# Optimization experiments

Hardware: AMD Instinct MI355X
Metric: run time of the kernel (lower is better)

## Reference

```python
import jax, jax.numpy as jnp
import numpy as np
from jax import lax

NPOINT, RADIUS, NSAMPLE, EPS = 2048, 0.1, 32, 1e-5


def setup_inputs() -> dict:
    key = jax.random.key(0)
    ks = jax.random.split(key, 8)
    B, N, D, CIN, COUT, DEPTH = 4, 8192, 29, 32, 64, 2
    return {
        "xyz": jax.random.uniform(ks[0], (B, 3, N), jnp.float32),
        "points": jax.random.normal(ks[1], (B, D, N), jnp.float32),
        "proj_w": jax.random.normal(ks[2], (COUT, CIN), jnp.float32) * 0.05,
        "proj_g": jnp.ones((COUT,), jnp.float32),
        "proj_b": jnp.zeros((COUT,), jnp.float32),
        "w1": jax.random.normal(ks[3], (DEPTH, COUT, COUT), jnp.float32) * 0.05,
        "g1": jnp.ones((DEPTH, COUT), jnp.float32),
        "b1": jnp.zeros((DEPTH, COUT), jnp.float32),
        "w2": jax.random.normal(ks[4], (DEPTH, COUT, COUT), jnp.float32) * 0.05,
        "g2": jnp.ones((DEPTH, COUT), jnp.float32),
        "b2": jnp.zeros((DEPTH, COUT), jnp.float32),
    }


def fps(xyz, npoint):
    # xyz: [B,N,3] -> idx [B,npoint]; deterministic start at index 0
    B, N, _ = xyz.shape
    def body(carry, _):
        dist, far = carry  # [B,N], [B]
        centroid = jnp.take_along_axis(xyz, far[:, None, None], axis=1)  # [B,1,3]
        d = jnp.sum((xyz - centroid) ** 2, -1)
        dist = jnp.minimum(dist, d)
        return (dist, jnp.argmax(dist, -1).astype(jnp.int32)), far
    init = (jnp.full((B, N), 1e10, xyz.dtype), jnp.zeros((B,), jnp.int32))
    _, idx = lax.scan(body, init, None, length=npoint)
    return jnp.transpose(idx)  # [B,npoint]


def ball_query(radius, nsample, xyz, new_xyz):
    # matches torch query_ball_point: invalid -> N, sort, take first nsample, backfill
    N = xyz.shape[1]
    sqr = (jnp.sum(new_xyz ** 2, -1)[:, :, None]
           + jnp.sum(xyz ** 2, -1)[:, None, :]
           - 2.0 * jnp.einsum("bsc,bnc->bsn", new_xyz, xyz))  # [B,S,N]
    cand = jnp.where(sqr <= radius * radius, jnp.arange(N, dtype=jnp.int32), jnp.int32(N))
    neg, _ = lax.top_k(-cand, nsample)
    idx = -neg  # nsample smallest indices, ascending
    first = idx[:, :, :1]
    return jnp.where(idx == N, first, idx)  # [B,S,K]


def gather_nb(p, idx):
    # p [B,N,C], idx [B,S,K] -> [B,S,K,C]
    return jax.vmap(lambda pb, ib: pb[ib])(p, idx)


def _conv(x, w):
    # 1x1 conv: w [O,C], x [B,C,K,S]
    return jnp.einsum("oc,bcks->boks", w, x)


def _bn(x, g, b):
    # training-mode BatchNorm2d over (B,K,S) per channel
    m = jnp.mean(x, (0, 2, 3), keepdims=True)
    v = jnp.var(x, (0, 2, 3), keepdims=True)
    return g[None, :, None, None] * (x - m) * lax.rsqrt(v + EPS) + b[None, :, None, None]


def reference(xyz, points, proj_w, proj_g, proj_b, w1, g1, b1, w2, g2, b2):
    xyz_t = jnp.transpose(xyz, (0, 2, 1))      # [B,N,3]
    pts_t = jnp.transpose(points, (0, 2, 1))   # [B,N,D]
    fidx = fps(xyz_t, NPOINT)                  # [B,S]
    new_xyz = jnp.take_along_axis(xyz_t, fidx[:, :, None], axis=1)  # [B,S,3]
    idx = ball_query(RADIUS, NSAMPLE, xyz_t, new_xyz)               # [B,S,K]
    grouped_xyz = gather_nb(xyz_t, idx) - new_xyz[:, :, None, :]    # [B,S,K,3]
    grouped_pts = gather_nb(pts_t, idx)                             # [B,S,K,D]
    new_points = jnp.concatenate([grouped_xyz, grouped_pts], -1)    # [B,S,K,3+D]
    x = jnp.transpose(new_points, (0, 3, 2, 1))                     # [B,C,K,S]
    x = jax.nn.relu(_bn(_conv(x, proj_w), proj_g, proj_b))
    for d in range(w1.shape[0]):
        idn = x
        x = jax.nn.relu(_bn(_conv(x, w1[d]), g1[d], b1[d]))
        x = _bn(_conv(x, w2[d]), g2[d], b2[d])
        x = jax.nn.relu(x + idn)
    feat = jnp.max(x, axis=2)                  # [B,Cout,S]
    return jnp.transpose(new_xyz, (0, 2, 1)), feat
```

## Files before the change

kernel.cpp:

```cpp
#include <hip/hip_runtime.h>
#include <cstdint>
#include <cstddef>

#define NPTS    8192
#define NPT     2048
#define KNB     32
#define NB      4
#define DPTS    29
#define CINP    32
#define CO      64
#define KS      (KNB*NPT)
#define TELEM   ((size_t)NB*CO*KS)
#define MCNT    262144.0f
#define BNEPS   1e-5f
#define FTHR    512
#define FWAVES  (FTHR/64)
#define FPT     16

typedef float v2f __attribute__((ext_vector_type(2)));

#define FPS_PAIR(P, A, B)                                                     \
    {                                                                         \
        v2f dx_, dy_, dz_, xx_, yy_, zz_, ss_, dd_;                           \
        asm("v_pk_add_f32 %0, %1, %2" : "=v"(dx_) : "v"(px##P), "v"(ncx));    \
        asm("v_pk_add_f32 %0, %1, %2" : "=v"(dy_) : "v"(py##P), "v"(ncy));    \
        asm("v_pk_add_f32 %0, %1, %2" : "=v"(dz_) : "v"(pz##P), "v"(ncz));    \
        asm("v_pk_mul_f32 %0, %1, %1" : "=v"(xx_) : "v"(dx_));                \
        asm("v_pk_mul_f32 %0, %1, %1" : "=v"(yy_) : "v"(dy_));                \
        asm("v_pk_mul_f32 %0, %1, %1" : "=v"(zz_) : "v"(dz_));                \
        asm("v_pk_add_f32 %0, %1, %2" : "=v"(ss_) : "v"(xx_), "v"(yy_));      \
        asm("v_pk_add_f32 %0, %1, %2" : "=v"(dd_) : "v"(ss_), "v"(zz_));      \
        d##A = fminf(d##A, dd_.x);                                            \
        d##B = fminf(d##B, dd_.y);                                            \
    }

static __device__ __forceinline__ unsigned long long umax64(unsigned long long a,
                                                            unsigned long long b) {
    return a > b ? a : b;
}

__global__ __launch_bounds__(FTHR) void fps_kernel(const float* __restrict__ xyz,
                                                   float* __restrict__ out0) {
    const int b = blockIdx.x;
    const int t = threadIdx.x;
    const int lane = t & 63;
    const int wid  = t >> 6;
    const float* xb = xyz + (size_t)b * 3 * NPTS;
    const int base = t * FPT;

    extern __shared__ float smem[];
    float* sx = smem;
    float* sy = sx + NPTS;
    float* sz = sy + NPTS;
    float* sc = sz + NPTS;
    unsigned long long* skey = (unsigned long long*)(sc + 3 * NPT);

    v2f px0,px1,px2,px3,px4,px5,px6,px7;
    v2f py0,py1,py2,py3,py4,py5,py6,py7;
    v2f pz0,pz1,pz2,pz3,pz4,pz5,pz6,pz7;
    float d0,d1,d2,d3,d4,d5,d6,d7,d8,d9,d10,d11,d12,d13,d14,d15;
    {
        const float4* x4 = (const float4*)(xb + base);
        const float4* y4 = (const float4*)(xb + NPTS + base);
        const float4* z4 = (const float4*)(xb + 2 * NPTS + base);
        float4* lx4 = (float4*)(sx + base);
        float4* ly4 = (float4*)(sy + base);
        float4* lz4 = (float4*)(sz + base);
        float4 v;
        v = x4[0]; lx4[0] = v; px0 = (v2f){v.x, v.y}; px1 = (v2f){v.z, v.w};
        v = x4[1]; lx4[1] = v; px2 = (v2f){v.x, v.y}; px3 = (v2f){v.z, v.w};
        v = x4[2]; lx4[2] = v; px4 = (v2f){v.x, v.y}; px5 = (v2f){v.z, v.w};
        v = x4[3]; lx4[3] = v; px6 = (v2f){v.x, v.y}; px7 = (v2f){v.z, v.w};
        v = y4[0]; ly4[0] = v; py0 = (v2f){v.x, v.y}; py1 = (v2f){v.z, v.w};
        v = y4[1]; ly4[1] = v; py2 = (v2f){v.x, v.y}; py3 = (v2f){v.z, v.w};
        v = y4[2]; ly4[2] = v; py4 = (v2f){v.x, v.y}; py5 = (v2f){v.z, v.w};
        v = y4[3]; ly4[3] = v; py6 = (v2f){v.x, v.y}; py7 = (v2f){v.z, v.w};
        v = z4[0]; lz4[0] = v; pz0 = (v2f){v.x, v.y}; pz1 = (v2f){v.z, v.w};
        v = z4[1]; lz4[1] = v; pz2 = (v2f){v.x, v.y}; pz3 = (v2f){v.z, v.w};
        v = z4[2]; lz4[2] = v; pz4 = (v2f){v.x, v.y}; pz5 = (v2f){v.z, v.w};
        v = z4[3]; lz4[3] = v; pz6 = (v2f){v.x, v.y}; pz7 = (v2f){v.z, v.w};
        d0=d1=d2=d3=d4=d5=d6=d7=d8=d9=d10=d11=d12=d13=d14=d15 = 1e10f;
    }

    float cx = xb[0], cy = xb[NPTS], cz = xb[2 * NPTS];
    float* ob = out0 + (size_t)b * 3 * NPT;
    if (t == 0) { sc[0] = cx; sc[NPT] = cy; sc[2 * NPT] = cz; }

    for (int i = 1; i < NPT; ++i) {
        const v2f ncx = (v2f){-cx, -cx};
        const v2f ncy = (v2f){-cy, -cy};
        const v2f ncz = (v2f){-cz, -cz};
        FPS_PAIR(0, 0, 1)   FPS_PAIR(1, 2, 3)
        FPS_PAIR(2, 4, 5)   FPS_PAIR(3, 6, 7)
        FPS_PAIR(4, 8, 9)   FPS_PAIR(5, 10, 11)
        FPS_PAIR(6, 12, 13) FPS_PAIR(7, 14, 15)

        float m0 = fmaxf(fmaxf(d0,  d1),  d2);
        float m1 = fmaxf(fmaxf(d3,  d4),  d5);
        float m2 = fmaxf(fmaxf(d6,  d7),  d8);
        float m3 = fmaxf(fmaxf(d9,  d10), d11);
        float m4 = fmaxf(fmaxf(d12, d13), d14);
        float u0 = fmaxf(fmaxf(m0, m1), m2);
        float u1 = fmaxf(fmaxf(m3, m4), d15);
        float tb = fmaxf(u0, u1);

        unsigned q0 = ((d0  == tb) ? 0x0001u : 0u) | ((d1  == tb) ? 0x0002u : 0u);
        unsigned q1 = ((d2  == tb) ? 0x0004u : 0u) | ((d3  == tb) ? 0x0008u : 0u);
        unsigned q2 = ((d4  == tb) ? 0x0010u : 0u) | ((d5  == tb) ? 0x0020u : 0u);
        unsigned q3 = ((d6  == tb) ? 0x0040u : 0u) | ((d7  == tb) ? 0x0080u : 0u);
        unsigned q4 = ((d8  == tb) ? 0x0100u : 0u) | ((d9  == tb) ? 0x0200u : 0u);
        unsigned q5 = ((d10 == tb) ? 0x0400u : 0u) | ((d11 == tb) ? 0x0800u : 0u);
        unsigned q6 = ((d12 == tb) ? 0x1000u : 0u) | ((d13 == tb) ? 0x2000u : 0u);
        unsigned q7 = ((d14 == tb) ? 0x4000u : 0u) | ((d15 == tb) ? 0x8000u : 0u);
        unsigned mk = (q0 | q1) | (q2 | q3) | (q4 | q5) | (q6 | q7);
        const int jj = __builtin_ctz(mk);
        const int gidx = base + jj;

        float r = tb;
        asm volatile(
            "s_nop 1\n\t"
            "v_max_f32 %0, %0, %0 row_shr:1\n\t"
            "s_nop 1\n\t"
            "v_max_f32 %0, %0, %0 row_shr:2\n\t"
            "s_nop 1\n\t"
            "v_max_f32 %0, %0, %0 row_shr:4\n\t"
            "s_nop 1\n\t"
            "v_max_f32 %0, %0, %0 row_shr:8\n\t"
            "s_nop 1\n\t"
            "v_max_f32 %0, %0, %0 row_bcast:15 row_mask:0xa\n\t"
            "s_nop 1\n\t"
            "v_max_f32 %0, %0, %0 row_bcast:31 row_mask:0xc\n\t"
            "s_nop 1"
            : "+v"(r));
        const float wm = __uint_as_float(
            (unsigned int)__builtin_amdgcn_readlane((int)__float_as_uint(r), 63));

        unsigned long long eq = __ballot(tb == wm);
        const int lwin = __ffsll((long long)eq) - 1;
        const int wgid = __builtin_amdgcn_readlane(gidx, lwin);

        const int par = i & 1;
        if (lane == 0)
            skey[par * FWAVES + wid] =
                (((unsigned long long)__float_as_uint(wm)) << 32) |
                (unsigned int)(~(unsigned int)wgid);
        __syncthreads();

        const ulonglong2* sk2 = (const ulonglong2*)(skey + par * FWAVES);
        ulonglong2 k01 = sk2[0], k23 = sk2[1], k45 = sk2[2], k67 = sk2[3];
        unsigned long long ka = umax64(k01.x, k01.y);
        unsigned long long kb = umax64(k23.x, k23.y);
        unsigned long long kc = umax64(k45.x, k45.y);
        unsigned long long kd = umax64(k67.x, k67.y);
        unsigned long long kbest = umax64(umax64(ka, kb), umax64(kc, kd));
        const int widx = (int)(~(unsigned int)kbest);

        cx = sx[widx]; cy = sy[widx]; cz = sz[widx];
        if (t == 0) { sc[i] = cx; sc[NPT + i] = cy; sc[2 * NPT + i] = cz; }
    }

    __syncthreads();
    const float4* s4 = (const float4*)sc;
    float4* o4 = (float4*)ob;
#pragma unroll
    for (int k = 0; k < 3; ++k) o4[t + k * FTHR] = s4[t + k * FTHR];
}

__global__ __launch_bounds__(256) void ballq_kernel(const float* __restrict__ xyz,
                                                    const float* __restrict__ out0,
                                                    int* __restrict__ idx) {
    const int gw   = (blockIdx.x * 256 + threadIdx.x) >> 6;
    const int lane = threadIdx.x & 63;
    const int b  = gw >> 11;
    const int si = gw & 2047;
    const float* xb = xyz + (size_t)b * 3 * NPTS;

    const float cx = out0[b * 3 * NPT + si];
    const float cy = out0[b * 3 * NPT + NPT + si];
    const float cz = out0[b * 3 * NPT + 2*NPT + si];
    const float csum = __fadd_rn(__fadd_rn(__fmul_rn(cx, cx), __fmul_rn(cy, cy)),
                                 __fmul_rn(cz, cz));
    const float R2 = (float)(0.1 * 0.1);

    __shared__ int buf[4][KNB];
    int* mybuf = buf[threadIdx.x >> 6];

    int cnt = 0;
    for (int n0 = 0; n0 < NPTS && cnt < KNB; n0 += 64) {
        const int i = n0 + lane;
        float pxv = xb[i], pyv = xb[NPTS + i], pzv = xb[2 * NPTS + i];
        float ps = __fadd_rn(__fadd_rn(__fmul_rn(pxv, pxv), __fmul_rn(pyv, pyv)),
                             __fmul_rn(pzv, pzv));
        float dot = __fmaf_rn(pzv, cz, __fmaf_rn(pyv, cy, __fmul_rn(pxv, cx)));
        float sqr = __fsub_rn(__fadd_rn(csum, ps), __fadd_rn(dot, dot));
        bool hit = (sqr <= R2);
        unsigned long long m = __ballot(hit);
        int pos = cnt + __popcll(m & ((1ull << lane) - 1ull));
        if (hit && pos < KNB) mybuf[pos] = i;
        cnt += __popcll(m);
    }
    int c = cnt < KNB ? cnt : KNB;
    int first = (cnt > 0) ? mybuf[0] : 0;
    if (lane < KNB) {
        int v = (lane < c) ? mybuf[lane] : first;
        idx[((size_t)gw << 5) + lane] = v;
    }
}

__global__ __launch_bounds__(256) void proj_kernel(const float* __restrict__ xyz,
                                                   const float* __restrict__ points,
                                                   const float* __restrict__ out0,
                                                   const int* __restrict__ idx,
                                                   const float* __restrict__ W,
                                                   float* __restrict__ out,
                                                   float* __restrict__ stats) {
    const int p = blockIdx.x * 256 + threadIdx.x;
    const int b = p >> 16;
    const int q = p & 65535;
    const int k = q >> 11;
    const int s = q & 2047;
    const int tid = threadIdx.x;

    __shared__ float ssum[CO], ssq[CO];
    if (tid < CO) { ssum[tid] = 0.f; ssq[tid] = 0.f; }
    __syncthreads();

    const int j = idx[((size_t)(b * NPT + s) << 5) + k];
    const float* xb = xyz + (size_t)b * 3 * NPTS;
    float a[CINP];
    a[0] = xb[j]            - out0[b * 3 * NPT + s];
    a[1] = xb[NPTS + j]     - out0[b * 3 * NPT + NPT + s];
    a[2] = xb[2*NPTS + j]   - out0[b * 3 * NPT + 2*NPT + s];
    const float* pb = points + (size_t)b * DPTS * NPTS;
#pragma unroll
    for (int c = 0; c < DPTS; ++c) a[3 + c] = pb[c * NPTS + j];

    const size_t obase = (size_t)b * CO * KS + q;
    for (int o = 0; o < CO; ++o) {
        float acc = 0.f;
#pragma unroll
        for (int c = 0; c < CINP; ++c) acc = __fmaf_rn(W[o * CINP + c], a[c], acc);
        out[obase + (size_t)o * KS] = acc;
        float s1 = acc, s2 = acc * acc;
#pragma unroll
        for (int off = 32; off > 0; off >>= 1) {
            s1 += __shfl_xor(s1, off, 64);
            s2 += __shfl_xor(s2, off, 64);
        }
        if ((tid & 63) == 0) { atomicAdd(&ssum[o], s1); atomicAdd(&ssq[o], s2); }
    }
    __syncthreads();
    if (tid < CO) {
        atomicAdd(&stats[tid], ssum[tid]);
        atomicAdd(&stats[CO + tid], ssq[tid]);
    }
}

template <bool HAS_IDN, bool WRITE_ACT>
__global__ __launch_bounds__(256) void conv_bn_kernel(const float* in,
                                                      const float* idn,
                                                      const float* __restrict__ stats_in,
                                                      const float* __restrict__ gamma,
                                                      const float* __restrict__ beta,
                                                      const float* __restrict__ W,
                                                      float* act_out,
                                                      float* out,
                                                      float* __restrict__ stats_out) {
    const int p = blockIdx.x * 256 + threadIdx.x;
    const int b = p >> 16;
    const int q = p & 65535;
    const int tid = threadIdx.x;

    __shared__ float ssc[CO], ssh[CO], ssum[CO], ssq[CO];
    if (tid < CO) {
        const float Minv = 1.0f / MCNT;
        float m = stats_in[tid] * Minv;
        float v = stats_in[CO + tid] * Minv - m * m;
        float scl = gamma[tid] * rsqrtf(v + BNEPS);
        ssc[tid] = scl;
        ssh[tid] = beta[tid] - m * scl;
        ssum[tid] = 0.f; ssq[tid] = 0.f;
    }
    __syncthreads();

    const size_t base = (size_t)b * CO * KS + q;
    float a[CO];
#pragma unroll
    for (int c = 0; c < CO; ++c) {
        float v = __fmaf_rn(ssc[c], in[base + (size_t)c * KS], ssh[c]);
        if (HAS_IDN) v += idn[base + (size_t)c * KS];
        v = fmaxf(v, 0.0f);
        a[c] = v;
        if (WRITE_ACT) act_out[base + (size_t)c * KS] = v;
    }
    for (int o = 0; o < CO; ++o) {
        float acc = 0.f;
#pragma unroll
        for (int c = 0; c < CO; ++c) acc = __fmaf_rn(W[o * CO + c], a[c], acc);
        out[base + (size_t)o * KS] = acc;
        float s1 = acc, s2 = acc * acc;
#pragma unroll
        for (int off = 32; off > 0; off >>= 1) {
            s1 += __shfl_xor(s1, off, 64);
            s2 += __shfl_xor(s2, off, 64);
        }
        if ((tid & 63) == 0) { atomicAdd(&ssum[o], s1); atomicAdd(&ssq[o], s2); }
    }
    __syncthreads();
    if (tid < CO) {
        atomicAdd(&stats_out[tid], ssum[tid]);
        atomicAdd(&stats_out[CO + tid], ssq[tid]);
    }
}

__global__ __launch_bounds__(256) void final_kernel(const float* __restrict__ y2,
                                                    const float* __restrict__ idn,
                                                    const float* __restrict__ stats,
                                                    const float* __restrict__ gamma,
                                                    const float* __restrict__ beta,
                                                    float* __restrict__ feat) {
    const int p = blockIdx.x * 256 + threadIdx.x;
    const int s = p & 2047;
    const int o = (p >> 11) & 63;
    const int b = p >> 17;
    const float Minv = 1.0f / MCNT;
    float m = stats[o] * Minv;
    float v = stats[CO + o] * Minv - m * m;
    float scl = gamma[o] * rsqrtf(v + BNEPS);
    float sh  = beta[o] - m * scl;
    const size_t base = (size_t)b * CO * KS + (size_t)o * KS + s;
    float mx = -1e30f;
#pragma unroll
    for (int k = 0; k < KNB; ++k) {
        float val = __fmaf_rn(scl, y2[base + (size_t)k * NPT], sh) + idn[base + (size_t)k * NPT];
        val = fmaxf(val, 0.0f);
        mx = fmaxf(mx, val);
    }
    feat[p] = mx;
}

__global__ void zero_kernel(float* p, int n) {
    int i = blockIdx.x * blockDim.x + threadIdx.x;
    if (i < n) p[i] = 0.f;
}

extern "C" void kernel_launch(void* const* d_in, const int* in_sizes, int n_in,
                              void* d_out, int out_size, void* d_ws, size_t ws_size,
                              hipStream_t stream) {
    (void)in_sizes; (void)n_in; (void)out_size; (void)ws_size;
    const float* xyz    = (const float*)d_in[0];
    const float* points = (const float*)d_in[1];
    const float* proj_w = (const float*)d_in[2];
    const float* proj_g = (const float*)d_in[3];
    const float* proj_b = (const float*)d_in[4];
    const float* w1     = (const float*)d_in[5];
    const float* g1     = (const float*)d_in[6];
    const float* b1     = (const float*)d_in[7];
    const float* w2     = (const float*)d_in[8];
    const float* g2     = (const float*)d_in[9];
    const float* b2     = (const float*)d_in[10];

    float* out0 = (float*)d_out;
    float* feat = (float*)d_out + NB * 3 * NPT;

    float* stats = (float*)d_ws;
    int*   idx   = (int*)((float*)d_ws + 1024);
    float* A     = (float*)(idx + NB * NPT * KNB);
    float* B     = A + TELEM;

    const size_t fps_lds = (size_t)(3 * NPTS + 3 * NPT) * sizeof(float)
                         + 2 * FWAVES * sizeof(unsigned long long);

    hipLaunchKernelGGL(zero_kernel, dim3(3), dim3(256), 0, stream, stats, 5 * 2 * CO);
    hipLaunchKernelGGL(fps_kernel, dim3(NB), dim3(FTHR), fps_lds, stream, xyz, out0);
    hipLaunchKernelGGL(ballq_kernel, dim3(2048), dim3(256), 0, stream, xyz, out0, idx);
    hipLaunchKernelGGL(proj_kernel, dim3(1024), dim3(256), 0, stream,
                       xyz, points, out0, idx, proj_w, A, stats);
    hipLaunchKernelGGL((conv_bn_kernel<false, true>), dim3(1024), dim3(256), 0, stream,
                       A, (const float*)nullptr, stats, proj_g, proj_b, w1,
                       B, A, stats + 128);
    hipLaunchKernelGGL((conv_bn_kernel<false, false>), dim3(1024), dim3(256), 0, stream,
                       A, (const float*)nullptr, stats + 128, g1, b1, w2,
                       (float*)nullptr, A, stats + 256);
    hipLaunchKernelGGL((conv_bn_kernel<true, true>), dim3(1024), dim3(256), 0, stream,
                       A, B, stats + 256, g2, b2, w1 + CO * CO,
                       B, A, stats + 384);
    hipLaunchKernelGGL((conv_bn_kernel<false, false>), dim3(1024), dim3(256), 0, stream,
                       A, (const float*)nullptr, stats + 384, g1 + CO, b1 + CO, w2 + CO * CO,
                       (float*)nullptr, A, stats + 512);
    hipLaunchKernelGGL(final_kernel, dim3(2048), dim3(256), 0, stream,
                       A, B, stats + 512, g2 + CO, b2 + CO, feat);
}
```

Measured before the change: 2.546 ms.

## Double FPS block to 1024 threads with 8 points per thread

The farthest-point-sampling kernel now runs 1024 threads per block, each owning 8 points instead of 16, so each thread does half the serial distance work in the 2047-iteration loop. The running max is folded into the per-pair update, and the argmin-index search becomes a select chain instead of a bitmask plus ctz. In exchange, the cross-wave reduction reads 16 wave keys instead of 8, and the block-wide barrier each iteration spans twice as many waves. The output copy loop is generalized so it works with the new thread count.

New measurement: 2.892 ms. 1.14x slower.

```diff
diff --git a/kernel.cpp b/kernel.cpp
--- a/kernel.cpp
+++ b/kernel.cpp
@@ -13,9 +13,9 @@
 #define TELEM   ((size_t)NB*CO*KS)
 #define MCNT    262144.0f
 #define BNEPS   1e-5f
-#define FTHR    512
+#define FTHR    1024
 #define FWAVES  (FTHR/64)
-#define FPT     16
+#define FPT     8
 
 typedef float v2f __attribute__((ext_vector_type(2)));
 
@@ -30,8 +30,9 @@
         asm("v_pk_mul_f32 %0, %1, %1" : "=v"(zz_) : "v"(dz_));                \
         asm("v_pk_add_f32 %0, %1, %2" : "=v"(ss_) : "v"(xx_), "v"(yy_));      \
         asm("v_pk_add_f32 %0, %1, %2" : "=v"(dd_) : "v"(ss_), "v"(zz_));      \
-        d##A = fminf(d##A, dd_.x);                                            \
-        d##B = fminf(d##B, dd_.y);                                            \
+        float ndA = fminf(d##A, dd_.x);  d##A = ndA;                          \
+        float ndB = fminf(d##B, dd_.y);  d##B = ndB;                          \
+        tb = fmaxf(fmaxf(tb, ndA), ndB);                                      \
     }
 
 static __device__ __forceinline__ unsigned long long umax64(unsigned long long a,
@@ -55,10 +56,10 @@
     float* sc = sz + NPTS;
     unsigned long long* skey = (unsigned long long*)(sc + 3 * NPT);
 
-    v2f px0,px1,px2,px3,px4,px5,px6,px7;
-    v2f py0,py1,py2,py3,py4,py5,py6,py7;
-    v2f pz0,pz1,pz2,pz3,pz4,pz5,pz6,pz7;
-    float d0,d1,d2,d3,d4,d5,d6,d7,d8,d9,d10,d11,d12,d13,d14,d15;
+    v2f px0,px1,px2,px3;
+    v2f py0,py1,py2,py3;
+    v2f pz0,pz1,pz2,pz3;
+    float d0,d1,d2,d3,d4,d5,d6,d7;
     {
         const float4* x4 = (const float4*)(xb + base);
         const float4* y4 = (const float4*)(xb + NPTS + base);
@@ -69,17 +70,11 @@
         float4 v;
         v = x4[0]; lx4[0] = v; px0 = (v2f){v.x, v.y}; px1 = (v2f){v.z, v.w};
         v = x4[1]; lx4[1] = v; px2 = (v2f){v.x, v.y}; px3 = (v2f){v.z, v.w};
-        v = x4[2]; lx4[2] = v; px4 = (v2f){v.x, v.y}; px5 = (v2f){v.z, v.w};
-        v = x4[3]; lx4[3] = v; px6 = (v2f){v.x, v.y}; px7 = (v2f){v.z, v.w};
         v = y4[0]; ly4[0] = v; py0 = (v2f){v.x, v.y}; py1 = (v2f){v.z, v.w};
         v = y4[1]; ly4[1] = v; py2 = (v2f){v.x, v.y}; py3 = (v2f){v.z, v.w};
-        v = y4[2]; ly4[2] = v; py4 = (v2f){v.x, v.y}; py5 = (v2f){v.z, v.w};
-        v = y4[3]; ly4[3] = v; py6 = (v2f){v.x, v.y}; py7 = (v2f){v.z, v.w};
         v = z4[0]; lz4[0] = v; pz0 = (v2f){v.x, v.y}; pz1 = (v2f){v.z, v.w};
         v = z4[1]; lz4[1] = v; pz2 = (v2f){v.x, v.y}; pz3 = (v2f){v.z, v.w};
-        v = z4[2]; lz4[2] = v; pz4 = (v2f){v.x, v.y}; pz5 = (v2f){v.z, v.w};
-        v = z4[3]; lz4[3] = v; pz6 = (v2f){v.x, v.y}; pz7 = (v2f){v.z, v.w};
-        d0=d1=d2=d3=d4=d5=d6=d7=d8=d9=d10=d11=d12=d13=d14=d15 = 1e10f;
+        d0=d1=d2=d3=d4=d5=d6=d7 = 1e10f;
     }
 
     float cx = xb[0], cy = xb[NPTS], cz = xb[2 * NPTS];
@@ -90,30 +85,19 @@
         const v2f ncx = (v2f){-cx, -cx};
         const v2f ncy = (v2f){-cy, -cy};
         const v2f ncz = (v2f){-cz, -cz};
+        float tb = -1.0f;
         FPS_PAIR(0, 0, 1)   FPS_PAIR(1, 2, 3)
         FPS_PAIR(2, 4, 5)   FPS_PAIR(3, 6, 7)
-        FPS_PAIR(4, 8, 9)   FPS_PAIR(5, 10, 11)
-        FPS_PAIR(6, 12, 13) FPS_PAIR(7, 14, 15)
-
-        float m0 = fmaxf(fmaxf(d0,  d1),  d2);
-        float m1 = fmaxf(fmaxf(d3,  d4),  d5);
-        float m2 = fmaxf(fmaxf(d6,  d7),  d8);
-        float m3 = fmaxf(fmaxf(d9,  d10), d11);
-        float m4 = fmaxf(fmaxf(d12, d13), d14);
-        float u0 = fmaxf(fmaxf(m0, m1), m2);
-        float u1 = fmaxf(fmaxf(m3, m4), d15);
-        float tb = fmaxf(u0, u1);
-
-        unsigned q0 = ((d0  == tb) ? 0x0001u : 0u) | ((d1  == tb) ? 0x0002u : 0u);
-        unsigned q1 = ((d2  == tb) ? 0x0004u : 0u) | ((d3  == tb) ? 0x0008u : 0u);
-        unsigned q2 = ((d4  == tb) ? 0x0010u : 0u) | ((d5  == tb) ? 0x0020u : 0u);
-        unsigned q3 = ((d6  == tb) ? 0x0040u : 0u) | ((d7  == tb) ? 0x0080u : 0u);
-        unsigned q4 = ((d8  == tb) ? 0x0100u : 0u) | ((d9  == tb) ? 0x0200u : 0u);
-        unsigned q5 = ((d10 == tb) ? 0x0400u : 0u) | ((d11 == tb) ? 0x0800u : 0u);
-        unsigned q6 = ((d12 == tb) ? 0x1000u : 0u) | ((d13 == tb) ? 0x2000u : 0u);
-        unsigned q7 = ((d14 == tb) ? 0x4000u : 0u) | ((d15 == tb) ? 0x8000u : 0u);
-        unsigned mk = (q0 | q1) | (q2 | q3) | (q4 | q5) | (q6 | q7);
-        const int jj = __builtin_ctz(mk);
+
+        int jj = 0;
+        jj = (d7 == tb) ? 7 : jj;
+        jj = (d6 == tb) ? 6 : jj;
+        jj = (d5 == tb) ? 5 : jj;
+        jj = (d4 == tb) ? 4 : jj;
+        jj = (d3 == tb) ? 3 : jj;
+        jj = (d2 == tb) ? 2 : jj;
+        jj = (d1 == tb) ? 1 : jj;
+        jj = (d0 == tb) ? 0 : jj;
         const int gidx = base + jj;
 
         float r = tb;
@@ -148,10 +132,11 @@
 
         const ulonglong2* sk2 = (const ulonglong2*)(skey + par * FWAVES);
         ulonglong2 k01 = sk2[0], k23 = sk2[1], k45 = sk2[2], k67 = sk2[3];
-        unsigned long long ka = umax64(k01.x, k01.y);
-        unsigned long long kb = umax64(k23.x, k23.y);
-        unsigned long long kc = umax64(k45.x, k45.y);
-        unsigned long long kd = umax64(k67.x, k67.y);
+        ulonglong2 k89 = sk2[4], kab = sk2[5], kcd = sk2[6], kef = sk2[7];
+        unsigned long long ka = umax64(umax64(k01.x, k01.y), umax64(k23.x, k23.y));
+        unsigned long long kb = umax64(umax64(k45.x, k45.y), umax64(k67.x, k67.y));
+        unsigned long long kc = umax64(umax64(k89.x, k89.y), umax64(kab.x, kab.y));
+        unsigned long long kd = umax64(umax64(kcd.x, kcd.y), umax64(kef.x, kef.y));
         unsigned long long kbest = umax64(umax64(ka, kb), umax64(kc, kd));
         const int widx = (int)(~(unsigned int)kbest);
 
@@ -162,8 +147,7 @@
     __syncthreads();
     const float4* s4 = (const float4*)sc;
     float4* o4 = (float4*)ob;
-#pragma unroll
-    for (int k = 0; k < 3; ++k) o4[t + k * FTHR] = s4[t + k * FTHR];
+    for (int e = t; e < 3 * NPT / 4; e += FTHR) o4[e] = s4[e];
 }
 
 __global__ __launch_bounds__(256) void ballq_kernel(const float* __restrict__ xyz,
```
